# Performance work log

Hardware: AMD Instinct MI355X
Metric: run time of the kernel (lower is better)

## Reference

```python
import jax, jax.numpy as jnp
import numpy as np

PRIOR_SCALE = 0.1
LOG_PS = float(np.log(PRIOR_SCALE))
NEG_SLOPE = 0.01  # nn.LeakyReLU default


def _kl_mean(mu, log_sigma, axes):
    # kl_div(mu_q, lsq, 0, lsp) = lsp - lsq + (exp(lsq)^2 + mu^2)/(2*exp(lsp)^2) - 0.5, mean over param dims
    kl = LOG_PS - log_sigma + (jnp.exp(log_sigma) ** 2 + mu ** 2) / (2.0 * PRIOR_SCALE ** 2) - 0.5
    return jnp.mean(kl, axis=axes)  # -> per-feature [F]


def _bayes_linear(x, wmu, wls, bmu, bls, ew, eb):
    # x: [B,F,Din], wmu/wls/ew: [F,Din,Dout], bmu/bls/eb: [F,Dout]
    W = wmu + jnp.exp(wls) * ew
    b = bmu + jnp.exp(bls) * eb
    out = jnp.einsum('bfi,fio->bfo', x, W) + b[None, :, :]
    kl_f = _kl_mean(wmu, wls, (1, 2)) + _kl_mean(bmu, bls, (1,))  # [F]
    return out, kl_f


def setup_inputs() -> dict:
    key = jax.random.key(0)
    ks = jax.random.split(key, 20)
    B, F, H = 16384, 64, 64
    inp = {
        'f': jax.random.normal(ks[0], (B, F), jnp.float32),
        'wmu0': jax.random.normal(ks[1], (F, 1, H), jnp.float32),
        'wls0': jax.random.normal(ks[2], (F, 1, H), jnp.float32),
        'bmu0': jax.random.normal(ks[3], (F, H), jnp.float32),
        'bls0': jax.random.normal(ks[4], (F, H), jnp.float32),
        'ew0': jax.random.normal(ks[5], (F, 1, H), jnp.float32),
        'eb0': jax.random.normal(ks[6], (F, H), jnp.float32),
        'wmu1': jax.random.normal(ks[7], (F, H, H), jnp.float32),
        'wls1': jax.random.normal(ks[8], (F, H, H), jnp.float32),
        'bmu1': jax.random.normal(ks[9], (F, H), jnp.float32),
        'bls1': jax.random.normal(ks[10], (F, H), jnp.float32),
        'ew1': jax.random.normal(ks[11], (F, H, H), jnp.float32),
        'eb1': jax.random.normal(ks[12], (F, H), jnp.float32),
        'wmu2': jax.random.normal(ks[13], (F, H, 1), jnp.float32),
        'wls2': jax.random.normal(ks[14], (F, H, 1), jnp.float32),
        'bmu2': jax.random.normal(ks[15], (F, 1), jnp.float32),
        'bls2': jax.random.normal(ks[16], (F, 1), jnp.float32),
        'ew2': jax.random.normal(ks[17], (F, H, 1), jnp.float32),
        'eb2': jax.random.normal(ks[18], (F, 1), jnp.float32),
        'bias': jnp.zeros((1,), jnp.float32),
    }
    return inp


def reference(f, wmu0, wls0, bmu0, bls0, ew0, eb0,
              wmu1, wls1, bmu1, bls1, ew1, eb1,
              wmu2, wls2, bmu2, bls2, ew2, eb2, bias):
    x = f[:, :, None]  # [B,F,1] (per-feature scalar input)
    out, kl0 = _bayes_linear(x, wmu0, wls0, bmu0, bls0, ew0, eb0)
    out = jax.nn.leaky_relu(out, NEG_SLOPE)
    out, kl1 = _bayes_linear(out, wmu1, wls1, bmu1, bls1, ew1, eb1)
    out = jax.nn.leaky_relu(out, NEG_SLOPE)  # dropout p=0 -> identity
    out, kl2 = _bayes_linear(out, wmu2, wls2, bmu2, bls2, ew2, eb2)  # [B,F,1]
    kl_total = jnp.sum(kl0 + kl1 + kl2)  # sum over features of per-feature kl sums
    conc = out[:, :, 0]  # concat of per-feature scalar outputs -> [B,F]
    y = jnp.sum(conc, axis=-1) + bias[0]  # feature_dropout p=0 -> identity
    return y, kl_total
```

## Files before the change

kernel.cpp:

```cpp
#include <hip/hip_runtime.h>
#include <hip/hip_fp16.h>

typedef _Float16 f16x8 __attribute__((ext_vector_type(8)));
typedef _Float16 f16x4 __attribute__((ext_vector_type(4)));
typedef _Float16 f16x2 __attribute__((ext_vector_type(2)));
typedef __fp16   fp16v2 __attribute__((ext_vector_type(2)));
typedef float floatx4 __attribute__((ext_vector_type(4)));

#define NEG 0.01f
#define KL_C (-2.8025850929940457f)

#define W0HOFF 131072
#define B0HOFF 133120
#define B1OFF  135168
#define W2HOFF 139264
#define B2OFF  143360
#define KLPOFF 143424

__device__ __forceinline__ f16x2 cvt2(float a, float b) {
    union { fp16v2 p; f16x2 h; } u;
    u.p = __builtin_amdgcn_cvt_pkrtz(a, b);
    return u.h;
}

__device__ __forceinline__ float wave_red(float v) {
    v += __shfl_xor(v, 1, 64);  v += __shfl_xor(v, 2, 64);
    v += __shfl_xor(v, 4, 64);  v += __shfl_xor(v, 8, 64);
    v += __shfl_xor(v, 16, 64); v += __shfl_xor(v, 32, 64);
    return v;
}

__global__ void bayesnam_prep(const float* __restrict__ wmu0, const float* __restrict__ wls0,
                              const float* __restrict__ bmu0, const float* __restrict__ bls0,
                              const float* __restrict__ ew0,  const float* __restrict__ eb0,
                              const float* __restrict__ wmu1, const float* __restrict__ wls1,
                              const float* __restrict__ bmu1, const float* __restrict__ bls1,
                              const float* __restrict__ ew1,  const float* __restrict__ eb1,
                              const float* __restrict__ wmu2, const float* __restrict__ wls2,
                              const float* __restrict__ bmu2, const float* __restrict__ bls2,
                              const float* __restrict__ ew2,  const float* __restrict__ eb2,
                              const float* __restrict__ bias,
                              float* __restrict__ ws, float* __restrict__ out) {
    const int tid = threadIdx.x;
    const int bx  = blockIdx.x;
    __shared__ float red[4];
    if (bx < 512) {
        const int f = bx >> 3;
        const int g = bx & 7;
        __shared__ float w1s[8 * 65];
        const size_t base = (size_t)f * 4096 + (size_t)g * 512;
        float klacc = 0.f;
        #pragma unroll
        for (int i = 0; i < 2; ++i) {
            const int idx = i * 256 + tid;
            const float m = wmu1[base + idx];
            const float l = wls1[base + idx];
            const float e = ew1[base + idx];
            const float ex = expf(l);
            w1s[(idx >> 6) * 65 + (idx & 63)] = fmaf(ex, e, m);
            klacc += (KL_C - l) + 50.f * fmaf(ex, ex, m * m);
        }
        const float wv = wave_red(klacc * 0.000244140625f);
        if ((tid & 63) == 0) red[tid >> 6] = wv;
        __syncthreads();
        if (tid == 0) ws[KLPOFF + bx] = red[0] + red[1] + red[2] + red[3];
        if (tid < 64) {
            const int n   = tid >> 4;
            const int l15 = tid & 15;
            const int kk  = g >> 2;
            const int lg  = g & 3;
            const int col = n * 16 + l15;
            union { _Float16 h[8]; uint4 u; } fr;
            #pragma unroll
            for (int j = 0; j < 8; ++j) fr.h[j] = (_Float16)w1s[j * 65 + col];
            ((uint4*)ws)[(size_t)f * 512 + kk * 256 + n * 64 + lg * 16 + l15] = fr.u;
        }
    } else {
        float klacc = 0.f;
        _Float16* w0h = (_Float16*)(ws + W0HOFF);
        _Float16* b0h = (_Float16*)(ws + B0HOFF);
        _Float16* w2h = (_Float16*)(ws + W2HOFF);
        for (int idx = (bx - 512) * 256 + tid; idx < 16448; idx += 2048) {
            const float *mu, *ls, *ew;
            int j, kind; float scale;
            if (idx < 4096)       { j = idx;         mu = wmu0; ls = wls0; ew = ew0; scale = 0.015625f; kind = 0; }
            else if (idx < 8192)  { j = idx - 4096;  mu = bmu0; ls = bls0; ew = eb0; scale = 0.015625f; kind = 1; }
            else if (idx < 12288) { j = idx - 8192;  mu = bmu1; ls = bls1; ew = eb1; scale = 0.015625f; kind = 2; }
            else if (idx < 16384) { j = idx - 12288; mu = wmu2; ls = wls2; ew = ew2; scale = 0.015625f; kind = 3; }
            else                  { j = idx - 16384; mu = bmu2; ls = bls2; ew = eb2; scale = 1.0f;      kind = 4; }
            const float m = mu[j], l = ls[j], e = ew[j];
            const float ex = expf(l);
            const float w  = fmaf(ex, e, m);
            if (kind == 0)      w0h[j] = (_Float16)w;
            else if (kind == 1) b0h[j] = (_Float16)w;
            else if (kind == 2) ws[B1OFF + j] = w;
            else if (kind == 3) {
                const int h = j & 63;
                w2h[(j & ~63) | ((h >> 5) << 5) | ((h & 15) << 1) | ((h >> 4) & 1)] = (_Float16)w;
            }
            else                ws[B2OFF + j] = w;
            klacc += scale * ((KL_C - l) + 50.f * fmaf(ex, ex, m * m));
        }
        const float bv = bias[0];
        for (int i = (bx - 512) * 256 + tid; i < 16384; i += 2048) out[i] = bv;
        const float wv = wave_red(klacc);
        if ((tid & 63) == 0) red[tid >> 6] = wv;
        __syncthreads();
        if (tid == 0) ws[KLPOFF + 512 + (bx - 512)] = red[0] + red[1] + red[2] + red[3];
    }
}

__global__ __launch_bounds__(256, 3) void bayesnam_main(const float* __restrict__ fin,
                                                        const float* __restrict__ ws,
                                                        float* __restrict__ out) {
    __shared__ uint4 fragLDS[2048];
    __shared__ __align__(16) float pLDS[644];
    const int tid = threadIdx.x;
    const int l   = tid & 63;
    const int wid = tid >> 6;
    const int l15 = l & 15;
    const int lg  = l >> 4;
    const int rowbase = blockIdx.x * 256 + wid * 64;
    const int f0 = blockIdx.y * 4;

    {
        const char* gsrc = (const char*)ws + (size_t)f0 * 8192;
        #pragma unroll
        for (int i = 0; i < 8; ++i) {
            const int chunk = (wid * 8 + i) * 1024;
            __builtin_amdgcn_global_load_lds(
                (const __attribute__((address_space(1))) unsigned int*)(gsrc + chunk + l * 16),
                (__attribute__((address_space(3))) unsigned int*)((char*)fragLDS + chunk),
                16, 0, 0);
        }
    }
    {
        if (tid < 128)      pLDS[tid]       = (ws + W0HOFF + f0 * 32)[tid];
        else                pLDS[tid]       = (ws + B0HOFF + f0 * 32)[tid - 128];
        pLDS[256 + tid] = (ws + B1OFF + f0 * 64)[tid];
        if (tid < 128)      pLDS[512 + tid] = (ws + W2HOFF + f0 * 32)[tid];
        if (tid < 4)        pLDS[640 + tid] = ws[B2OFF + f0 + tid];
    }

    if (blockIdx.x == 0 && blockIdx.y == 0 && tid < 64) {
        float k = 0.f;
        #pragma unroll
        for (int i = 0; i < 9; ++i) {
            const int p = tid + i * 64;
            if (p < 520) k += ws[KLPOFF + p];
        }
        k += __shfl_xor(k, 32, 64); k += __shfl_xor(k, 16, 64); k += __shfl_xor(k, 8, 64);
        k += __shfl_xor(k, 4, 64);  k += __shfl_xor(k, 2, 64);  k += __shfl_xor(k, 1, 64);
        if (tid == 0) out[16384] = k;
    }

    const f16x2 neg2 = {(_Float16)0.01f, (_Float16)0.01f};

    f16x4 xh[4];
    #pragma unroll
    for (int rt = 0; rt < 4; ++rt) {
        const floatx4 xv = *(const floatx4*)(fin + (size_t)(rowbase + rt * 16 + l15) * 64 + f0);
        xh[rt] = f16x4{(_Float16)xv[0], (_Float16)xv[1], (_Float16)xv[2], (_Float16)xv[3]};
    }

    __syncthreads();

    const _Float16* __restrict__ ph = (const _Float16*)pLDS;

    f16x2 ypk[4][4];
    #pragma unroll
    for (int rt = 0; rt < 4; ++rt)
        #pragma unroll
        for (int q = 0; q < 4; ++q) ypk[rt][q] = f16x2{(_Float16)0.f, (_Float16)0.f};
    float b2sum = 0.f;

    #pragma unroll 1
    for (int fi = 0; fi < 4; ++fi) {
        floatx4 acc[4][4];
        #pragma unroll
        for (int n = 0; n < 4; ++n) {
            const float bv = pLDS[256 + fi * 64 + n * 16 + l15];
            #pragma unroll
            for (int rt = 0; rt < 4; ++rt) acc[rt][n] = floatx4{bv, bv, bv, bv};
        }

        #pragma unroll
        for (int kk = 0; kk < 2; ++kk) {
            const int kb = kk * 32 + lg * 8;
            union HU { uint4 u; f16x8 v; } wu, bu, bf[4];
            wu.u = *(const uint4*)(ph + fi * 64 + kb);
            bu.u = *(const uint4*)(ph + 256 + fi * 64 + kb);
            #pragma unroll
            for (int n = 0; n < 4; ++n) bf[n].u = fragLDS[(fi * 8 + kk * 4 + n) * 64 + l];

            #pragma unroll
            for (int rt = 0; rt < 4; ++rt) {
                const _Float16 xs = xh[rt][fi];
                f16x8 t = wu.v * xs + bu.v;
                f16x8 a = __builtin_elementwise_max(t, t * neg2[0]);
                #pragma unroll
                for (int n = 0; n < 4; ++n)
                    acc[rt][n] = __builtin_amdgcn_mfma_f32_16x16x32_f16(a, bf[n].v, acc[rt][n], 0, 0, 0);
            }
        }

        const f16x2 w2p0 = *(const f16x2*)(ph + 1024 + fi * 64 + l15 * 2);
        const f16x2 w2p1 = *(const f16x2*)(ph + 1024 + fi * 64 + 32 + l15 * 2);
        #pragma unroll
        for (int rt = 0; rt < 4; ++rt)
            #pragma unroll
            for (int q = 0; q < 4; ++q) {
                f16x2 h0 = cvt2(acc[rt][0][q], acc[rt][1][q]);
                f16x2 h1 = cvt2(acc[rt][2][q], acc[rt][3][q]);
                f16x2 lk0 = __builtin_elementwise_max(h0, h0 * neg2);
                f16x2 lk1 = __builtin_elementwise_max(h1, h1 * neg2);
                ypk[rt][q] = lk0 * w2p0 + ypk[rt][q];
                ypk[rt][q] = lk1 * w2p1 + ypk[rt][q];
            }
        b2sum += pLDS[640 + fi];
    }

    #pragma unroll
    for (int rt = 0; rt < 4; ++rt)
        #pragma unroll
        for (int q = 0; q < 4; ++q) {
            float v = (float)ypk[rt][q][0] + (float)ypk[rt][q][1];
            v += __shfl_xor(v, 1, 64);
            v += __shfl_xor(v, 2, 64);
            v += __shfl_xor(v, 4, 64);
            v += __shfl_xor(v, 8, 64);
            if (l15 == 0)
                atomicAdd(&out[rowbase + rt * 16 + lg * 4 + q], v + b2sum);
        }
}

extern "C" void kernel_launch(void* const* d_in, const int* in_sizes, int n_in,
                              void* d_out, int out_size, void* d_ws, size_t ws_size,
                              hipStream_t stream) {
    const float* fin  = (const float*)d_in[0];
    const float* wmu0 = (const float*)d_in[1];
    const float* wls0 = (const float*)d_in[2];
    const float* bmu0 = (const float*)d_in[3];
    const float* bls0 = (const float*)d_in[4];
    const float* ew0  = (const float*)d_in[5];
    const float* eb0  = (const float*)d_in[6];
    const float* wmu1 = (const float*)d_in[7];
    const float* wls1 = (const float*)d_in[8];
    const float* bmu1 = (const float*)d_in[9];
    const float* bls1 = (const float*)d_in[10];
    const float* ew1  = (const float*)d_in[11];
    const float* eb1  = (const float*)d_in[12];
    const float* wmu2 = (const float*)d_in[13];
    const float* wls2 = (const float*)d_in[14];
    const float* bmu2 = (const float*)d_in[15];
    const float* bls2 = (const float*)d_in[16];
    const float* ew2  = (const float*)d_in[17];
    const float* eb2  = (const float*)d_in[18];
    const float* bias = (const float*)d_in[19];

    float* ws  = (float*)d_ws;
    float* out = (float*)d_out;

    hipLaunchKernelGGL(bayesnam_prep, dim3(520), dim3(256), 0, stream,
                       wmu0, wls0, bmu0, bls0, ew0, eb0,
                       wmu1, wls1, bmu1, bls1, ew1, eb1,
                       wmu2, wls2, bmu2, bls2, ew2, eb2,
                       bias, ws, out);

    hipLaunchKernelGGL(bayesnam_main, dim3(64, 16), dim3(256), 0, stream,
                       fin, ws, out);
}
```

Baseline: 27.06 us.

## Halve features per block and split hidden columns to raise occupancy

Each block now handles two features instead of four, doubling the grid to 64x32. LDS staging shrinks to match, and the output-column loop is split into two halves so only 4x2 accumulators are live at once. Launch bounds go from 3 to 4 blocks per CU. This trades lower register and LDS pressure and more parallel blocks for twice as many atomic adds on the output and more redundant loads of the input rows.

```diff
diff --git a/kernel.cpp b/kernel.cpp
--- a/kernel.cpp
+++ b/kernel.cpp
@@ -2,10 +2,10 @@
 #include <hip/hip_fp16.h>
 
 typedef _Float16 f16x8 __attribute__((ext_vector_type(8)));
-typedef _Float16 f16x4 __attribute__((ext_vector_type(4)));
 typedef _Float16 f16x2 __attribute__((ext_vector_type(2)));
 typedef __fp16   fp16v2 __attribute__((ext_vector_type(2)));
 typedef float floatx4 __attribute__((ext_vector_type(4)));
+typedef float floatx2 __attribute__((ext_vector_type(2)));
 
 #define NEG 0.01f
 #define KL_C (-2.8025850929940457f)
@@ -110,24 +110,24 @@
     }
 }
 
-__global__ __launch_bounds__(256, 3) void bayesnam_main(const float* __restrict__ fin,
+__global__ __launch_bounds__(256, 4) void bayesnam_main(const float* __restrict__ fin,
                                                         const float* __restrict__ ws,
                                                         float* __restrict__ out) {
-    __shared__ uint4 fragLDS[2048];
-    __shared__ __align__(16) float pLDS[644];
+    __shared__ uint4 fragLDS[1024];
+    __shared__ __align__(16) float pLDS[322];
     const int tid = threadIdx.x;
     const int l   = tid & 63;
     const int wid = tid >> 6;
     const int l15 = l & 15;
     const int lg  = l >> 4;
     const int rowbase = blockIdx.x * 256 + wid * 64;
-    const int f0 = blockIdx.y * 4;
+    const int f0 = blockIdx.y * 2;
 
     {
         const char* gsrc = (const char*)ws + (size_t)f0 * 8192;
         #pragma unroll
-        for (int i = 0; i < 8; ++i) {
-            const int chunk = (wid * 8 + i) * 1024;
+        for (int i = 0; i < 4; ++i) {
+            const int chunk = (wid * 4 + i) * 1024;
             __builtin_amdgcn_global_load_lds(
                 (const __attribute__((address_space(1))) unsigned int*)(gsrc + chunk + l * 16),
                 (__attribute__((address_space(3))) unsigned int*)((char*)fragLDS + chunk),
@@ -135,11 +135,11 @@
         }
     }
     {
-        if (tid < 128)      pLDS[tid]       = (ws + W0HOFF + f0 * 32)[tid];
-        else                pLDS[tid]       = (ws + B0HOFF + f0 * 32)[tid - 128];
-        pLDS[256 + tid] = (ws + B1OFF + f0 * 64)[tid];
-        if (tid < 128)      pLDS[512 + tid] = (ws + W2HOFF + f0 * 32)[tid];
-        if (tid < 4)        pLDS[640 + tid] = ws[B2OFF + f0 + tid];
+        if (tid < 64)                      pLDS[tid]       = (ws + W0HOFF + f0 * 32)[tid];
+        else if (tid < 128)                pLDS[tid]       = (ws + B0HOFF + f0 * 32)[tid - 64];
+        if (tid < 128)                     pLDS[128 + tid] = (ws + B1OFF + f0 * 64)[tid];
+        else if (tid < 192)                pLDS[128 + tid] = (ws + W2HOFF + f0 * 32)[tid - 128];
+        if (tid >= 192 && tid < 194)       pLDS[320 + (tid - 192)] = ws[B2OFF + f0 + (tid - 192)];
     }
 
     if (blockIdx.x == 0 && blockIdx.y == 0 && tid < 64) {
@@ -156,11 +156,11 @@
 
     const f16x2 neg2 = {(_Float16)0.01f, (_Float16)0.01f};
 
-    f16x4 xh[4];
+    f16x2 xh[4];
     #pragma unroll
     for (int rt = 0; rt < 4; ++rt) {
-        const floatx4 xv = *(const floatx4*)(fin + (size_t)(rowbase + rt * 16 + l15) * 64 + f0);
-        xh[rt] = f16x4{(_Float16)xv[0], (_Float16)xv[1], (_Float16)xv[2], (_Float16)xv[3]};
+        const floatx2 xv = *(const floatx2*)(fin + (size_t)(rowbase + rt * 16 + l15) * 64 + f0);
+        xh[rt] = f16x2{(_Float16)xv[0], (_Float16)xv[1]};
     }
 
     __syncthreads();
@@ -175,49 +175,49 @@
     float b2sum = 0.f;
 
     #pragma unroll 1
-    for (int fi = 0; fi < 4; ++fi) {
-        floatx4 acc[4][4];
-        #pragma unroll
-        for (int n = 0; n < 4; ++n) {
-            const float bv = pLDS[256 + fi * 64 + n * 16 + l15];
-            #pragma unroll
-            for (int rt = 0; rt < 4; ++rt) acc[rt][n] = floatx4{bv, bv, bv, bv};
-        }
-
-        #pragma unroll
-        for (int kk = 0; kk < 2; ++kk) {
-            const int kb = kk * 32 + lg * 8;
-            union HU { uint4 u; f16x8 v; } wu, bu, bf[4];
-            wu.u = *(const uint4*)(ph + fi * 64 + kb);
-            bu.u = *(const uint4*)(ph + 256 + fi * 64 + kb);
-            #pragma unroll
-            for (int n = 0; n < 4; ++n) bf[n].u = fragLDS[(fi * 8 + kk * 4 + n) * 64 + l];
-
-            #pragma unroll
-            for (int rt = 0; rt < 4; ++rt) {
-                const _Float16 xs = xh[rt][fi];
-                f16x8 t = wu.v * xs + bu.v;
-                f16x8 a = __builtin_elementwise_max(t, t * neg2[0]);
-                #pragma unroll
-                for (int n = 0; n < 4; ++n)
-                    acc[rt][n] = __builtin_amdgcn_mfma_f32_16x16x32_f16(a, bf[n].v, acc[rt][n], 0, 0, 0);
+    for (int fi = 0; fi < 2; ++fi) {
+        #pragma unroll 1
+        for (int nh = 0; nh < 2; ++nh) {
+            floatx4 acc[4][2];
+            #pragma unroll
+            for (int n2 = 0; n2 < 2; ++n2) {
+                const float bv = pLDS[128 + fi * 64 + (nh * 2 + n2) * 16 + l15];
+                #pragma unroll
+                for (int rt = 0; rt < 4; ++rt) acc[rt][n2] = floatx4{bv, bv, bv, bv};
             }
-        }
-
-        const f16x2 w2p0 = *(const f16x2*)(ph + 1024 + fi * 64 + l15 * 2);
-        const f16x2 w2p1 = *(const f16x2*)(ph + 1024 + fi * 64 + 32 + l15 * 2);
-        #pragma unroll
-        for (int rt = 0; rt < 4; ++rt)
-            #pragma unroll
-            for (int q = 0; q < 4; ++q) {
-                f16x2 h0 = cvt2(acc[rt][0][q], acc[rt][1][q]);
-                f16x2 h1 = cvt2(acc[rt][2][q], acc[rt][3][q]);
-                f16x2 lk0 = __builtin_elementwise_max(h0, h0 * neg2);
-                f16x2 lk1 = __builtin_elementwise_max(h1, h1 * neg2);
-                ypk[rt][q] = lk0 * w2p0 + ypk[rt][q];
-                ypk[rt][q] = lk1 * w2p1 + ypk[rt][q];
+
+            #pragma unroll
+            for (int kk = 0; kk < 2; ++kk) {
+                const int kb = kk * 32 + lg * 8;
+                union HU { uint4 u; f16x8 v; } wu, bu, bf[2];
+                wu.u = *(const uint4*)(ph + fi * 64 + kb);
+                bu.u = *(const uint4*)(ph + 128 + fi * 64 + kb);
+                #pragma unroll
+                for (int n2 = 0; n2 < 2; ++n2)
+                    bf[n2].u = fragLDS[(fi * 8 + kk * 4 + nh * 2 + n2) * 64 + l];
+
+                #pragma unroll
+                for (int rt = 0; rt < 4; ++rt) {
+                    const _Float16 xs = xh[rt][fi];
+                    f16x8 t = wu.v * xs + bu.v;
+                    f16x8 a = __builtin_elementwise_max(t, t * neg2[0]);
+                    #pragma unroll
+                    for (int n2 = 0; n2 < 2; ++n2)
+                        acc[rt][n2] = __builtin_amdgcn_mfma_f32_16x16x32_f16(a, bf[n2].v, acc[rt][n2], 0, 0, 0);
+                }
             }
-        b2sum += pLDS[640 + fi];
+
+            const f16x2 w2p = *(const f16x2*)(ph + 512 + fi * 64 + nh * 32 + l15 * 2);
+            #pragma unroll
+            for (int rt = 0; rt < 4; ++rt)
+                #pragma unroll
+                for (int q = 0; q < 4; ++q) {
+                    f16x2 h2 = cvt2(acc[rt][0][q], acc[rt][1][q]);
+                    f16x2 lk = __builtin_elementwise_max(h2, h2 * neg2);
+                    ypk[rt][q] = lk * w2p + ypk[rt][q];
+                }
+        }
+        b2sum += pLDS[320 + fi];
     }
 
     #pragma unroll
@@ -267,6 +267,6 @@
                        wmu2, wls2, bmu2, bls2, ew2, eb2,
                        bias, ws, out);
 
-    hipLaunchKernelGGL(bayesnam_main, dim3(64, 16), dim3(256), 0, stream,
+    hipLaunchKernelGGL(bayesnam_main, dim3(64, 32), dim3(256), 0, stream,
                        fin, ws, out);
 }
```

New measurement: 29.38 us. 1.09x slower.
